# Kernel optimization log

Hardware: AMD Instinct MI355X
Metric: run time of the kernel (lower is better)

## Reference

```python
import jax, jax.numpy as jnp
import numpy as np

S_DIM = 128            # attention head width s
E_DIM = 1024           # expansion e = 2*hidden
SQRT_S = 128.0 ** 0.5
EPS = 1e-5


def setup_inputs() -> dict:
    key = jax.random.key(0)
    ks = jax.random.split(key, 8)
    B, S, H = 64, 512, 512
    uv_dim = 2 * E_DIM + S_DIM  # 2176
    # xavier-uniform-ish scale for uv weight
    lim = (6.0 / (H + uv_dim)) ** 0.5
    return {
        "x": jax.random.normal(ks[0], (B, S, H), dtype=jnp.float32),
        "ln_g": jnp.ones((1,), dtype=jnp.float32),
        "uv_w": jax.random.uniform(ks[1], (uv_dim, H), minval=-lim, maxval=lim, dtype=jnp.float32),
        "uv_b": jnp.zeros((uv_dim,), dtype=jnp.float32),
        "gamma": jax.random.uniform(ks[2], (2, S_DIM), dtype=jnp.float32),
        "beta": jax.random.uniform(ks[3], (2, S_DIM), dtype=jnp.float32),
        "w_bias": jax.random.uniform(ks[4], (2 * S - 1,), dtype=jnp.float32),
        "o_w": jax.random.normal(ks[5], (H, E_DIM), dtype=jnp.float32) * 0.02,
        "o_b": jnp.zeros((H,), dtype=jnp.float32),
    }


def _rope(x):
    # x: [B, S, 2, s]; rotate along the sequence dim (dim=1)
    S = x.shape[1]
    half = x.shape[-1] // 2
    pos = jnp.arange(S, dtype=jnp.float32)
    # torch: freq_seq = -arange(half)/half; inv_freq = 10000**(-freq_seq)
    inv_freq = 10000.0 ** (jnp.arange(half, dtype=jnp.float32) / half)
    sinus = pos[:, None, None] * inv_freq[None, None, :]  # [S, 1, half]
    sin, cos = jnp.sin(sinus), jnp.cos(sinus)
    x1, x2 = x[..., :half], x[..., half:]
    return jnp.concatenate([x1 * cos - x2 * sin, x2 * cos + x1 * sin], axis=-1)


def reference(x, ln_g, uv_w, uv_b, gamma, beta, w_bias, o_w, o_b):
    B, S, H = x.shape
    # ScaleNorm
    norm = jnp.linalg.norm(x, axis=-1, keepdims=True) * (H ** -0.5)
    xn = x / jnp.maximum(norm, EPS) * ln_g
    # fused uv projection + SiLU
    act = jax.nn.silu(xn @ uv_w.T + uv_b)  # [B, S, 2e+s]
    u = act[..., :E_DIM]
    v = act[..., E_DIM:2 * E_DIM]
    base = act[..., 2 * E_DIM:]                      # [B, S, s]
    base = base[:, :, None, :] * gamma + beta        # [B, S, 2, s]
    base = _rope(base)
    q, k = base[:, :, 0, :], base[:, :, 1, :]
    # scores + relative position bias: bias[i, j] = w[j - i + S - 1]
    qk = jnp.einsum('bsd,btd->bst', q, k)
    idx = jnp.arange(S)[None, :] - jnp.arange(S)[:, None] + (S - 1)
    qk = qk + w_bias[idx]
    # relu2 similarity kernel
    kernel = jnp.square(jax.nn.relu(qk / SQRT_S))    # [B, S, S]
    out = u * jnp.einsum('bst,bte->bse', kernel, v)  # gated attention
    out = out @ o_w.T + o_b
    return out + x  # use_shortcut: hidden == output
```

## Files before the change

kernel.cpp:

```cpp
#include <hip/hip_runtime.h>
#include <math.h>


#define M_TOT   32768
#define S_LEN   512
#define H_DIM   512
#define E_DIMC  1024
#define UV_DIM  2176
#define UV_PAD  2304
#define D_DIM   128

using floatx4  = __attribute__((ext_vector_type(4))) float;
using uintx2   = __attribute__((ext_vector_type(2))) unsigned int;
using uintx4   = __attribute__((ext_vector_type(4))) unsigned int;
using ushortx4 = __attribute__((ext_vector_type(4))) unsigned short;
using short8   = __attribute__((ext_vector_type(8))) short;

#define ASYNC_CP16(gsrc, ldst)                                                  \
    __builtin_amdgcn_global_load_lds(                                           \
        (const __attribute__((address_space(1))) void*)(gsrc),                  \
        (__attribute__((address_space(3))) void*)(ldst), 16, 0, 0)

__device__ __forceinline__ float bf2f(unsigned short h) {
    union { unsigned int u; float f; } c;
    c.u = ((unsigned int)h) << 16;
    return c.f;
}
__device__ __forceinline__ unsigned short f2bf(float f) {
    union { float f; unsigned int u; } c;
    c.f = f;
    unsigned int r = c.u + 0x7fffu + ((c.u >> 16) & 1u);
    return (unsigned short)(r >> 16);
}
__device__ __forceinline__ float silu_fast(float x) {
    float e = __expf(-x);
    return x * __builtin_amdgcn_rcpf(1.0f + e);
}
__device__ __forceinline__ int xcd_remap(int b, int nwg) {
    return (b & 7) * (nwg >> 3) + (b >> 3);
}

__global__ __launch_bounds__(256) void f2bf_kernel(const float* __restrict__ in,
                                                   unsigned short* __restrict__ out,
                                                   int n4) {
    int i = blockIdx.x * 256 + threadIdx.x;
    if (i < n4) {
        floatx4 v = ((const floatx4*)in)[i];
        ushortx4 o;
        o.x = f2bf(v.x); o.y = f2bf(v.y); o.z = f2bf(v.z); o.w = f2bf(v.w);
        ((ushortx4*)out)[i] = o;
    }
}

__global__ __launch_bounds__(256) void f2bf_pad_kernel(const float* __restrict__ in,
                                                       unsigned short* __restrict__ out,
                                                       int n4_src, int n4_dst) {
    int i = blockIdx.x * 256 + threadIdx.x;
    if (i < n4_dst) {
        ushortx4 o;
        if (i < n4_src) {
            floatx4 v = ((const floatx4*)in)[i];
            o.x = f2bf(v.x); o.y = f2bf(v.y); o.z = f2bf(v.z); o.w = f2bf(v.w);
        } else {
            o.x = 0; o.y = 0; o.z = 0; o.w = 0;
        }
        ((ushortx4*)out)[i] = o;
    }
}

__global__ __launch_bounds__(256) void rmsnorm_kernel(const float* __restrict__ x,
                                                      const float* __restrict__ ln_g,
                                                      unsigned short* __restrict__ xn) {
    int row  = blockIdx.x * 4 + (threadIdx.x >> 6);
    int lane = threadIdx.x & 63;
    const float* xr = x + (size_t)row * H_DIM;
    floatx4 v0 = ((const floatx4*)xr)[lane];
    floatx4 v1 = ((const floatx4*)xr)[lane + 64];
    float ss = v0.x*v0.x + v0.y*v0.y + v0.z*v0.z + v0.w*v0.w
             + v1.x*v1.x + v1.y*v1.y + v1.z*v1.z + v1.w*v1.w;
    #pragma unroll
    for (int off = 32; off > 0; off >>= 1) ss += __shfl_xor(ss, off, 64);
    float norm = sqrtf(ss) * 0.044194173824159216f;
    float sc   = ln_g[0] / fmaxf(norm, 1e-5f);
    unsigned short* xo = xn + (size_t)row * H_DIM;
    ushortx4 o0, o1;
    o0.x = f2bf(v0.x * sc); o0.y = f2bf(v0.y * sc);
    o0.z = f2bf(v0.z * sc); o0.w = f2bf(v0.w * sc);
    o1.x = f2bf(v1.x * sc); o1.y = f2bf(v1.y * sc);
    o1.z = f2bf(v1.z * sc); o1.w = f2bf(v1.w * sc);
    ((ushortx4*)xo)[lane]      = o0;
    ((ushortx4*)xo)[lane + 64] = o1;
}

__global__ __launch_bounds__(64) void rope_table_kernel(float* __restrict__ cost,
                                                        float* __restrict__ sint) {
    int s = blockIdx.x;
    int j = threadIdx.x;
    float invf = (float)pow(10000.0, (double)j / 64.0);
    float ang  = (float)s * invf;
    double a   = (double)ang;
    cost[s * 64 + j] = (float)cos(a);
    sint[s * 64 + j] = (float)sin(a);
}

__global__ __launch_bounds__(256) void rope_apply_kernel(const float* __restrict__ base,
                                                         const float* __restrict__ gamma,
                                                         const float* __restrict__ beta,
                                                         const float* __restrict__ cost,
                                                         const float* __restrict__ sint,
                                                         unsigned short* __restrict__ q,
                                                         unsigned short* __restrict__ k) {
    int idx = blockIdx.x * 256 + threadIdx.x;
    int m = idx >> 6;
    int j = idx & 63;
    int s = m & (S_LEN - 1);
    float b1 = base[(size_t)m * D_DIM + j];
    float b2 = base[(size_t)m * D_DIM + 64 + j];
    float c  = cost[s * 64 + j];
    float sn = sint[s * 64 + j];
    float yq1 = b1 * gamma[j]       + beta[j];
    float yq2 = b2 * gamma[64 + j]  + beta[64 + j];
    float yk1 = b1 * gamma[128 + j] + beta[128 + j];
    float yk2 = b2 * gamma[192 + j] + beta[192 + j];
    q[(size_t)m * D_DIM + j]      = f2bf(yq1 * c - yq2 * sn);
    q[(size_t)m * D_DIM + 64 + j] = f2bf(yq2 * c + yq1 * sn);
    k[(size_t)m * D_DIM + j]      = f2bf(yk1 * c - yk2 * sn);
    k[(size_t)m * D_DIM + 64 + j] = f2bf(yk2 * c + yk1 * sn);
}

template <bool SWAPT>
__device__ __forceinline__ void gemm128_core(const unsigned short* __restrict__ A,
                                             const unsigned short* __restrict__ B,
                                             int lda, int ldb, int K,
                                             int m0, int n0,
                                             unsigned short (&st)[3][12288],
                                             floatx4 (&acc)[4][4]) {
    const int tid  = threadIdx.x;
    const int lane = tid & 63;
    const int wave = tid >> 6;
    const int quad = lane >> 4;
    const int l16  = lane & 15;
    const int wrow = (wave >> 2) * 64;
    const int wcol = (wave & 3) * 64;

    const int qa  = wave * 64 + lane;
    const int Ra  = qa >> 3;
    const int ca  = (qa & 7) ^ (Ra & 7);
    const int srA = 2 * Ra + (ca >> 2);
    const int scA = (ca & 3) * 8;
    const unsigned short* pa  = A + (size_t)(m0 + srA) * lda + scA;
    const unsigned short* pb0 = B + (size_t)(n0 + srA) * ldb + scA;
    const unsigned short* pb1 = pb0 + (size_t)128 * ldb;
    const int ldsA  = (wave * 64) * 8;
    const int ldsB0 = 4096 + (wave * 64) * 8;
    const int ldsB1 = 4096 + (512 + wave * 64) * 8;

    #pragma unroll
    for (int i = 0; i < 4; i++)
        #pragma unroll
        for (int j = 0; j < 4; j++) acc[i][j] = (floatx4){0.f, 0.f, 0.f, 0.f};

    const int NT = K >> 5;
    auto stage = [&](int buf, int t) {
        unsigned short* s = &st[buf][0];
        const int kt = t * 32;
        ASYNC_CP16(pa  + kt, s + ldsA);
        ASYNC_CP16(pb0 + kt, s + ldsB0);
        ASYNC_CP16(pb1 + kt, s + ldsB1);
    };
    stage(0, 0);
    stage(1, 1);

    int aoff[4], boff[4];
    #pragma unroll
    for (int mt = 0; mt < 4; mt++) {
        int r  = wrow + mt * 16 + l16;
        int Rr = r >> 1;
        int cp = (((r & 1) << 2) + quad) ^ (Rr & 7);
        aoff[mt] = Rr * 64 + cp * 8;
    }
    #pragma unroll
    for (int nt = 0; nt < 4; nt++) {
        int r  = wcol + nt * 16 + l16;
        int Rr = r >> 1;
        int cp = (((r & 1) << 2) + quad) ^ (Rr & 7);
        boff[nt] = 4096 + Rr * 64 + cp * 8;
    }

    int bc = 0, bs = 2;
    for (int t = 0; t < NT; ++t) {
        if (t < NT - 1) asm volatile("s_waitcnt vmcnt(3)" ::: "memory");
        else            asm volatile("s_waitcnt vmcnt(0)" ::: "memory");
        __builtin_amdgcn_sched_barrier(0);
        __builtin_amdgcn_s_barrier();
        __builtin_amdgcn_sched_barrier(0);
        if (t + 2 < NT) stage(bs, t + 2);

        const unsigned short* sb = &st[bc][0];
        short8 af[4], bf[4];
        #pragma unroll
        for (int mt = 0; mt < 4; mt++) {
            union { short8 s8; uintx4 u4; } fu;
            fu.u4 = *(const uintx4*)&sb[aoff[mt]];
            af[mt] = fu.s8;
        }
        #pragma unroll
        for (int nt = 0; nt < 4; nt++) {
            union { short8 s8; uintx4 u4; } fu;
            fu.u4 = *(const uintx4*)&sb[boff[nt]];
            bf[nt] = fu.s8;
        }
        __builtin_amdgcn_s_setprio(1);
        #pragma unroll
        for (int mt = 0; mt < 4; mt++)
            #pragma unroll
            for (int nt = 0; nt < 4; nt++)
                acc[mt][nt] = SWAPT
                    ? __builtin_amdgcn_mfma_f32_16x16x32_bf16(bf[nt], af[mt], acc[mt][nt], 0, 0, 0)
                    : __builtin_amdgcn_mfma_f32_16x16x32_bf16(af[mt], bf[nt], acc[mt][nt], 0, 0, 0);
        __builtin_amdgcn_s_setprio(0);

        bc = (bc == 2) ? 0 : bc + 1;
        bs = (bs == 2) ? 0 : bs + 1;
    }
}

union __align__(16) Lds3 {
    unsigned short st[3][12288];
    unsigned short T[128 * 256];
};

__global__ __launch_bounds__(512, 2) void gemm1_128_kernel(const unsigned short* __restrict__ xn,
                                                           const unsigned short* __restrict__ uvw,
                                                           const float* __restrict__ uvb,
                                                           unsigned short* __restrict__ u,
                                                           unsigned short* __restrict__ vT,
                                                           float* __restrict__ base) {
    __shared__ Lds3 lds;
    floatx4 acc[4][4];
    const int bl = blockIdx.y * 9 + blockIdx.x;
    const int lg = xcd_remap(bl, 9 * (M_TOT / 128));
    const int xb = lg % 9;
    const int m0 = (lg / 9) * 128;
    const int tid = threadIdx.x, lane = tid & 63, wave = tid >> 6;
    const int quad = lane >> 4, l16 = lane & 15;
    const int wrow = (wave >> 2) * 64, wcol = (wave & 3) * 64;

    if (xb < 4) {
        const int n0 = xb * 256;
        gemm128_core<true>(xn, uvw, H_DIM, H_DIM, H_DIM, m0, n0, lds.st, acc);
        __syncthreads();
        #pragma unroll
        for (int mt = 0; mt < 4; mt++) {
            int row = wrow + mt * 16 + l16;
            #pragma unroll
            for (int nt = 0; nt < 4; nt++) {
                int nl = wcol + nt * 16 + quad * 4;
                floatx4 b4 = *(const floatx4*)&uvb[n0 + nl];
                ushortx4 pk;
                #pragma unroll
                for (int r = 0; r < 4; r++)
                    pk[r] = f2bf(silu_fast(acc[mt][nt][r] + b4[r]));
                *(uintx2*)&lds.T[row * 256 + (((nl >> 3) ^ (row & 15)) << 3) + (nl & 7)] = *(uintx2*)&pk;
            }
        }
        __syncthreads();
        #pragma unroll
        for (int i = 0; i < 8; i++) {
            int idx = tid + i * 512;
            int row = idx >> 5, c16 = idx & 31;
            *(uintx4*)(u + (size_t)(m0 + row) * E_DIMC + n0 + c16 * 8) =
                *(const uintx4*)&lds.T[row * 256 + ((c16 ^ (row & 15)) << 3)];
        }
    } else if (xb < 8) {
        const int n0 = xb * 256;
        gemm128_core<false>(xn, uvw, H_DIM, H_DIM, H_DIM, m0, n0, lds.st, acc);
        __syncthreads();
        #pragma unroll
        for (int nt = 0; nt < 4; nt++) {
            int rowT = wcol + nt * 16 + l16;
            float bias = uvb[n0 + rowT];
            #pragma unroll
            for (int mt = 0; mt < 4; mt++) {
                int colT = wrow + mt * 16 + quad * 4;
                ushortx4 pk;
                #pragma unroll
                for (int r = 0; r < 4; r++)
                    pk[r] = f2bf(silu_fast(acc[mt][nt][r] + bias));
                *(uintx2*)&lds.T[rowT * 128 + (((colT >> 3) ^ (rowT & 15)) << 3) + (colT & 7)] = *(uintx2*)&pk;
            }
        }
        __syncthreads();
        const int b = m0 >> 9, sg0 = m0 & (S_LEN - 1), eg0 = n0 - E_DIMC;
        #pragma unroll
        for (int i = 0; i < 8; i++) {
            int idx = tid + i * 512;
            int e = idx >> 4, j = idx & 15;
            *(uintx4*)(vT + ((size_t)b * E_DIMC + eg0 + e) * S_LEN + sg0 + j * 8) =
                *(const uintx4*)&lds.T[e * 128 + ((j ^ (e & 15)) << 3)];
        }
    } else {
        const int n0 = 2048;
        gemm128_core<false>(xn, uvw, H_DIM, H_DIM, H_DIM, m0, n0, lds.st, acc);
        if ((wave & 3) < 2) {
            #pragma unroll
            for (int mt = 0; mt < 4; mt++) {
                int m = m0 + wrow + mt * 16 + quad * 4;
                #pragma unroll
                for (int nt = 0; nt < 4; nt++) {
                    int n = wcol + nt * 16 + l16;
                    float bias = uvb[2048 + n];
                    #pragma unroll
                    for (int r = 0; r < 4; r++)
                        base[(size_t)(m + r) * D_DIM + n] = silu_fast(acc[mt][nt][r] + bias);
                }
            }
        }
    }
}

__global__ __launch_bounds__(512, 2) void gemm_out128_kernel(const unsigned short* __restrict__ oe,
                                                             const unsigned short* __restrict__ ow,
                                                             const float* __restrict__ ob,
                                                             const float* __restrict__ x,
                                                             float* __restrict__ out) {
    __shared__ __align__(16) unsigned short st[3][12288];
    floatx4 acc[4][4];
    const int bl = blockIdx.y * 2 + blockIdx.x;
    const int lg = xcd_remap(bl, 2 * (M_TOT / 128));
    const int n0 = (lg & 1) * 256;
    const int m0 = (lg >> 1) * 128;
    gemm128_core<true>(oe, ow, E_DIMC, E_DIMC, E_DIMC, m0, n0, st, acc);

    const int tid = threadIdx.x, lane = tid & 63, wave = tid >> 6;
    const int quad = lane >> 4, l16 = lane & 15;
    const int wrow = (wave >> 2) * 64, wcol = (wave & 3) * 64;
    #pragma unroll
    for (int mt = 0; mt < 4; mt++) {
        int m = m0 + wrow + mt * 16 + l16;
        #pragma unroll
        for (int nt = 0; nt < 4; nt++) {
            int n = n0 + wcol + nt * 16 + quad * 4;
            size_t off = (size_t)m * H_DIM + n;
            floatx4 b4 = *(const floatx4*)&ob[n];
            floatx4 x4 = *(const floatx4*)&x[off];
            *(floatx4*)&out[off] = acc[mt][nt] + b4 + x4;
        }
    }
}

__global__ __launch_bounds__(512, 2) void gemm_pv128_kernel(const unsigned short* __restrict__ P,
                                                            const unsigned short* __restrict__ vT,
                                                            unsigned short* __restrict__ u) {
    __shared__ Lds3 lds;
    floatx4 acc[4][4];
    const int bl = (blockIdx.z * 4 + blockIdx.y) * 4 + blockIdx.x;
    const int lg = xcd_remap(bl, 1024);
    const int bx = lg & 3, by = (lg >> 2) & 3, bb = lg >> 4;
    const unsigned short* Pb  = P  + (size_t)bb * S_LEN * S_LEN;
    const unsigned short* vTb = vT + (size_t)bb * E_DIMC * S_LEN;
    const int m0 = bx * 128, n0 = by * 256;
    gemm128_core<true>(Pb, vTb, S_LEN, S_LEN, S_LEN, m0, n0, lds.st, acc);

    const int tid = threadIdx.x, lane = tid & 63, wave = tid >> 6;
    const int quad = lane >> 4, l16 = lane & 15;
    const int wrow = (wave >> 2) * 64, wcol = (wave & 3) * 64;
    __syncthreads();
    #pragma unroll
    for (int mt = 0; mt < 4; mt++) {
        int row = wrow + mt * 16 + l16;
        #pragma unroll
        for (int nt = 0; nt < 4; nt++) {
            int nl = wcol + nt * 16 + quad * 4;
            ushortx4 pk;
            #pragma unroll
            for (int r = 0; r < 4; r++) pk[r] = f2bf(acc[mt][nt][r]);
            *(uintx2*)&lds.T[row * 256 + (((nl >> 3) ^ (row & 15)) << 3) + (nl & 7)] = *(uintx2*)&pk;
        }
    }
    __syncthreads();
    #pragma unroll
    for (int i = 0; i < 8; i++) {
        int idx = tid + i * 512;
        int row = idx >> 5, c16 = idx & 31;
        size_t off = ((size_t)bb * S_LEN + m0 + row) * E_DIMC + n0 + c16 * 8;
        union { uintx4 u4; unsigned short s[8]; } tv, uv, ov;
        tv.u4 = *(const uintx4*)&lds.T[row * 256 + ((c16 ^ (row & 15)) << 3)];
        uv.u4 = *(const uintx4*)(u + off);
        #pragma unroll
        for (int jj = 0; jj < 8; jj++) ov.s[jj] = f2bf(bf2f(tv.s[jj]) * bf2f(uv.s[jj]));
        *(uintx4*)(u + off) = ov.u4;
    }
}

struct GemmLds {
    unsigned short As[128 * 64];
    unsigned short Bs[128 * 64];
};

template <bool SWAPT>
__device__ __forceinline__ void gemm_bt_core(const unsigned short* __restrict__ A,
                                             const unsigned short* __restrict__ B,
                                             int lda, int ldb, int K,
                                             int m0, int n0,
                                             GemmLds& lds, floatx4 (&acc)[4][4]) {
    const int tid  = threadIdx.x;
    const int lane = tid & 63;
    const int wave = tid >> 6;
    const int quad = lane >> 4;
    const int l16  = lane & 15;
    const int wm   = (wave >> 1) * 64;
    const int wn   = (wave & 1) * 64;
    const int lrow = lane >> 3;
    const int cgs  = ((lane & 7) ^ lrow) * 8;

    #pragma unroll
    for (int i = 0; i < 4; i++)
        #pragma unroll
        for (int j = 0; j < 4; j++) acc[i][j] = (floatx4){0.f, 0.f, 0.f, 0.f};

    for (int kt = 0; kt < K; kt += 64) {
        #pragma unroll
        for (int i = 0; i < 4; i++) {
            int r0 = wave * 32 + i * 8;
            const unsigned short* ga = A + (size_t)(m0 + r0 + lrow) * lda + kt + cgs;
            const unsigned short* gb = B + (size_t)(n0 + r0 + lrow) * ldb + kt + cgs;
            ASYNC_CP16(ga, &lds.As[r0 * 64]);
            ASYNC_CP16(gb, &lds.Bs[r0 * 64]);
        }
        __syncthreads();
        #pragma unroll
        for (int kk = 0; kk < 64; kk += 32) {
            short8 af[4], bf[4];
            const int pc = (kk + quad * 8) ^ ((l16 & 7) * 8);
            #pragma unroll
            for (int mt = 0; mt < 4; mt++) {
                int row = wm + mt * 16 + l16;
                union { short8 s8; uintx4 u4; } fu;
                fu.u4 = *(const uintx4*)&lds.As[row * 64 + pc];
                af[mt] = fu.s8;
            }
            #pragma unroll
            for (int nt = 0; nt < 4; nt++) {
                int row = wn + nt * 16 + l16;
                union { short8 s8; uintx4 u4; } fu;
                fu.u4 = *(const uintx4*)&lds.Bs[row * 64 + pc];
                bf[nt] = fu.s8;
            }
            #pragma unroll
            for (int mt = 0; mt < 4; mt++)
                #pragma unroll
                for (int nt = 0; nt < 4; nt++)
                    acc[mt][nt] = SWAPT
                        ? __builtin_amdgcn_mfma_f32_16x16x32_bf16(bf[nt], af[mt], acc[mt][nt], 0, 0, 0)
                        : __builtin_amdgcn_mfma_f32_16x16x32_bf16(af[mt], bf[nt], acc[mt][nt], 0, 0, 0);
        }
        __syncthreads();
    }
}

union LdsU {
    GemmLds g;
    unsigned short T[128 * 128];
};
__device__ __forceinline__ int swz(int row, int col) {
    return row * 128 + ((((col >> 3) ^ (row & 7)) << 3) | (col & 7));
}

__global__ __launch_bounds__(256) void gemm_qk_kernel(const unsigned short* __restrict__ q,
                                                      const unsigned short* __restrict__ k,
                                                      const float* __restrict__ wbias,
                                                      unsigned short* __restrict__ P) {
    __shared__ LdsU lds;
    floatx4 acc[4][4];
    const int bl = (blockIdx.z * 4 + blockIdx.y) * 4 + blockIdx.x;
    const int lg = xcd_remap(bl, 1024);
    const int bx = lg & 3, by = (lg >> 2) & 3, bz = lg >> 4;
    size_t boff = (size_t)bz * S_LEN * D_DIM;
    unsigned short* Pb = P + (size_t)bz * S_LEN * S_LEN;
    const int m0 = bx * 128, n0 = by * 128;
    gemm_bt_core<true>(q + boff, k + boff, D_DIM, D_DIM, D_DIM, m0, n0, lds.g, acc);

    const int tid = threadIdx.x, lane = tid & 63, wave = tid >> 6;
    const int quad = lane >> 4, l16 = lane & 15;
    const int wm = (wave >> 1) * 64, wn = (wave & 1) * 64;
    #pragma unroll
    for (int mt = 0; mt < 4; mt++) {
        int row = wm + mt * 16 + l16;
        int s   = m0 + row;
        #pragma unroll
        for (int nt = 0; nt < 4; nt++) {
            int nl = wn + nt * 16 + quad * 4;
            int t0 = n0 + nl;
            ushortx4 pk;
            #pragma unroll
            for (int r = 0; r < 4; r++) {
                float z = (acc[mt][nt][r] + wbias[t0 + r - s + (S_LEN - 1)]) * 0.08838834764831845f;
                z = fmaxf(z, 0.f);
                pk[r] = f2bf(z * z);
            }
            *(uintx2*)&lds.T[swz(row, nl)] = *(uintx2*)&pk;
        }
    }
    __syncthreads();
    #pragma unroll
    for (int i = 0; i < 8; i++) {
        int idx = tid + i * 256;
        int row = idx >> 4;
        int j   = idx & 15;
        *(uintx4*)(Pb + (size_t)(m0 + row) * S_LEN + n0 + j * 8) =
            *(const uintx4*)&lds.T[swz(row, j * 8)];
    }
}

extern "C" void kernel_launch(void* const* d_in, const int* in_sizes, int n_in,
                              void* d_out, int out_size, void* d_ws, size_t ws_size,
                              hipStream_t stream) {
    const float* x     = (const float*)d_in[0];
    const float* ln_g  = (const float*)d_in[1];
    const float* uv_w  = (const float*)d_in[2];
    const float* uv_b  = (const float*)d_in[3];
    const float* gamma = (const float*)d_in[4];
    const float* beta  = (const float*)d_in[5];
    const float* wbias = (const float*)d_in[6];
    const float* o_w   = (const float*)d_in[7];
    const float* o_b   = (const float*)d_in[8];
    float* out = (float*)d_out;

    char* ws = (char*)d_ws;
    size_t off = 0;
    auto alloc = [&](size_t bytes) {
        void* p = ws + off;
        off += (bytes + 255) & ~(size_t)255;
        return p;
    };
    unsigned short* u     = (unsigned short*)alloc((size_t)M_TOT * E_DIMC * 2);
    unsigned short* vT    = (unsigned short*)alloc((size_t)64 * E_DIMC * S_LEN * 2);
    unsigned short* xn    = (unsigned short*)alloc((size_t)M_TOT * H_DIM * 2);
    unsigned short* P     = xn;
    float*          base  = (float*)alloc((size_t)M_TOT * D_DIM * 4);
    unsigned short* q     = (unsigned short*)alloc((size_t)M_TOT * D_DIM * 2);
    unsigned short* k     = (unsigned short*)alloc((size_t)M_TOT * D_DIM * 2);
    float*          cost  = (float*)alloc((size_t)S_LEN * 64 * 4);
    float*          sint  = (float*)alloc((size_t)S_LEN * 64 * 4);
    unsigned short* uvwb  = (unsigned short*)alloc((size_t)UV_PAD * H_DIM * 2);
    unsigned short* owb   = (unsigned short*)alloc((size_t)H_DIM * E_DIMC * 2);
    (void)ws_size; (void)in_sizes; (void)n_in; (void)out_size;

    f2bf_pad_kernel<<<(UV_PAD * H_DIM / 4 + 255) / 256, 256, 0, stream>>>(
        uv_w, uvwb, UV_DIM * H_DIM / 4, UV_PAD * H_DIM / 4);
    f2bf_kernel<<<(H_DIM * E_DIMC / 4 + 255) / 256, 256, 0, stream>>>(o_w, owb, H_DIM * E_DIMC / 4);
    rope_table_kernel<<<S_LEN, 64, 0, stream>>>(cost, sint);

    rmsnorm_kernel<<<M_TOT / 4, 256, 0, stream>>>(x, ln_g, xn);

    gemm1_128_kernel<<<dim3(9, M_TOT / 128), 512, 0, stream>>>(xn, uvwb, uv_b, u, vT, base);

    rope_apply_kernel<<<M_TOT * 64 / 256, 256, 0, stream>>>(base, gamma, beta, cost, sint, q, k);

    gemm_qk_kernel<<<dim3(S_LEN / 128, S_LEN / 128, 64), 256, 0, stream>>>(q, k, wbias, P);

    gemm_pv128_kernel<<<dim3(S_LEN / 128, E_DIMC / 256, 64), 512, 0, stream>>>(P, vT, u);

    gemm_out128_kernel<<<dim3(H_DIM / 256, M_TOT / 128), 512, 0, stream>>>(u, owb, o_b, x, out);
}
```

Before: 365.8 us.

## Shrink GEMM LDS to double buffering and split epilogue staging into halves

The shared 128x256 GEMM core goes from a triple-buffered cp.async pipeline with two stages in flight to a double-buffered one that waits for all loads before each tile. The epilogue transpose buffers are halved, and each kernel now writes its output through LDS in two passes with extra barriers, so the union fits in two stage buffers. The aim is to cut LDS per block from 72KB to 48KB, which could let more blocks share a CU. The cost is less latency hiding, since the prefetch depth drops to one tile and every iteration drains vmcnt, plus extra synchronisation in the epilogue.

```diff
diff --git a/kernel.cpp b/kernel.cpp
--- a/kernel.cpp
+++ b/kernel.cpp
@@ -133,7 +133,7 @@
                                              const unsigned short* __restrict__ B,
                                              int lda, int ldb, int K,
                                              int m0, int n0,
-                                             unsigned short (&st)[3][12288],
+                                             unsigned short (&st)[2][12288],
                                              floatx4 (&acc)[4][4]) {
     const int tid  = threadIdx.x;
     const int lane = tid & 63;
@@ -169,7 +169,6 @@
         ASYNC_CP16(pb1 + kt, s + ldsB1);
     };
     stage(0, 0);
-    stage(1, 1);
 
     int aoff[4], boff[4];
     #pragma unroll
@@ -187,16 +186,14 @@
         boff[nt] = 4096 + Rr * 64 + cp * 8;
     }
 
-    int bc = 0, bs = 2;
     for (int t = 0; t < NT; ++t) {
-        if (t < NT - 1) asm volatile("s_waitcnt vmcnt(3)" ::: "memory");
-        else            asm volatile("s_waitcnt vmcnt(0)" ::: "memory");
+        asm volatile("s_waitcnt vmcnt(0)" ::: "memory");
         __builtin_amdgcn_sched_barrier(0);
         __builtin_amdgcn_s_barrier();
         __builtin_amdgcn_sched_barrier(0);
-        if (t + 2 < NT) stage(bs, t + 2);
-
-        const unsigned short* sb = &st[bc][0];
+        if (t + 1 < NT) stage((t + 1) & 1, t + 1);
+
+        const unsigned short* sb = &st[t & 1][0];
         short8 af[4], bf[4];
         #pragma unroll
         for (int mt = 0; mt < 4; mt++) {
@@ -219,15 +216,12 @@
                     ? __builtin_amdgcn_mfma_f32_16x16x32_bf16(bf[nt], af[mt], acc[mt][nt], 0, 0, 0)
                     : __builtin_amdgcn_mfma_f32_16x16x32_bf16(af[mt], bf[nt], acc[mt][nt], 0, 0, 0);
         __builtin_amdgcn_s_setprio(0);
-
-        bc = (bc == 2) ? 0 : bc + 1;
-        bs = (bs == 2) ? 0 : bs + 1;
-    }
-}
-
-union __align__(16) Lds3 {
-    unsigned short st[3][12288];
-    unsigned short T[128 * 256];
+    }
+}
+
+union __align__(16) Lds2 {
+    unsigned short st[2][12288];
+    unsigned short T2[16384];
 };
 
 __global__ __launch_bounds__(512, 2) void gemm1_128_kernel(const unsigned short* __restrict__ xn,
@@ -236,7 +230,7 @@
                                                            unsigned short* __restrict__ u,
                                                            unsigned short* __restrict__ vT,
                                                            float* __restrict__ base) {
-    __shared__ Lds3 lds;
+    __shared__ Lds2 lds;
     floatx4 acc[4][4];
     const int bl = blockIdx.y * 9 + blockIdx.x;
     const int lg = xcd_remap(bl, 9 * (M_TOT / 128));
@@ -251,53 +245,65 @@
         gemm128_core<true>(xn, uvw, H_DIM, H_DIM, H_DIM, m0, n0, lds.st, acc);
         __syncthreads();
         #pragma unroll
-        for (int mt = 0; mt < 4; mt++) {
-            int row = wrow + mt * 16 + l16;
-            #pragma unroll
-            for (int nt = 0; nt < 4; nt++) {
-                int nl = wcol + nt * 16 + quad * 4;
-                floatx4 b4 = *(const floatx4*)&uvb[n0 + nl];
-                ushortx4 pk;
+        for (int h = 0; h < 2; h++) {
+            if ((wave >> 2) == h) {
                 #pragma unroll
-                for (int r = 0; r < 4; r++)
-                    pk[r] = f2bf(silu_fast(acc[mt][nt][r] + b4[r]));
-                *(uintx2*)&lds.T[row * 256 + (((nl >> 3) ^ (row & 15)) << 3) + (nl & 7)] = *(uintx2*)&pk;
-            }
-        }
-        __syncthreads();
-        #pragma unroll
-        for (int i = 0; i < 8; i++) {
-            int idx = tid + i * 512;
-            int row = idx >> 5, c16 = idx & 31;
-            *(uintx4*)(u + (size_t)(m0 + row) * E_DIMC + n0 + c16 * 8) =
-                *(const uintx4*)&lds.T[row * 256 + ((c16 ^ (row & 15)) << 3)];
+                for (int mt = 0; mt < 4; mt++) {
+                    int row = mt * 16 + l16;
+                    #pragma unroll
+                    for (int nt = 0; nt < 4; nt++) {
+                        int nl = wcol + nt * 16 + quad * 4;
+                        floatx4 b4 = *(const floatx4*)&uvb[n0 + nl];
+                        ushortx4 pk;
+                        #pragma unroll
+                        for (int r = 0; r < 4; r++)
+                            pk[r] = f2bf(silu_fast(acc[mt][nt][r] + b4[r]));
+                        *(uintx2*)&lds.T2[row * 256 + (((nl >> 3) ^ (row & 15)) << 3) + (nl & 7)] = *(uintx2*)&pk;
+                    }
+                }
+            }
+            __syncthreads();
+            #pragma unroll
+            for (int i = 0; i < 4; i++) {
+                int idx = tid + i * 512;
+                int row = idx >> 5, c16 = idx & 31;
+                *(uintx4*)(u + (size_t)(m0 + h * 64 + row) * E_DIMC + n0 + c16 * 8) =
+                    *(const uintx4*)&lds.T2[row * 256 + ((c16 ^ (row & 15)) << 3)];
+            }
+            __syncthreads();
         }
     } else if (xb < 8) {
         const int n0 = xb * 256;
         gemm128_core<false>(xn, uvw, H_DIM, H_DIM, H_DIM, m0, n0, lds.st, acc);
         __syncthreads();
-        #pragma unroll
-        for (int nt = 0; nt < 4; nt++) {
-            int rowT = wcol + nt * 16 + l16;
-            float bias = uvb[n0 + rowT];
-            #pragma unroll
-            for (int mt = 0; mt < 4; mt++) {
-                int colT = wrow + mt * 16 + quad * 4;
-                ushortx4 pk;
+        const int b = m0 >> 9, sg0 = m0 & (S_LEN - 1), eg0 = n0 - E_DIMC;
+        #pragma unroll
+        for (int h = 0; h < 2; h++) {
+            if (((wave & 3) >> 1) == h) {
                 #pragma unroll
-                for (int r = 0; r < 4; r++)
-                    pk[r] = f2bf(silu_fast(acc[mt][nt][r] + bias));
-                *(uintx2*)&lds.T[rowT * 128 + (((colT >> 3) ^ (rowT & 15)) << 3) + (colT & 7)] = *(uintx2*)&pk;
-            }
-        }
-        __syncthreads();
-        const int b = m0 >> 9, sg0 = m0 & (S_LEN - 1), eg0 = n0 - E_DIMC;
-        #pragma unroll
-        for (int i = 0; i < 8; i++) {
-            int idx = tid + i * 512;
-            int e = idx >> 4, j = idx & 15;
-            *(uintx4*)(vT + ((size_t)b * E_DIMC + eg0 + e) * S_LEN + sg0 + j * 8) =
-                *(const uintx4*)&lds.T[e * 128 + ((j ^ (e & 15)) << 3)];
+                for (int nt = 0; nt < 4; nt++) {
+                    int rowL = (wave & 1) * 64 + nt * 16 + l16;
+                    float bias = uvb[n0 + h * 128 + rowL];
+                    #pragma unroll
+                    for (int mt = 0; mt < 4; mt++) {
+                        int colT = wrow + mt * 16 + quad * 4;
+                        ushortx4 pk;
+                        #pragma unroll
+                        for (int r = 0; r < 4; r++)
+                            pk[r] = f2bf(silu_fast(acc[mt][nt][r] + bias));
+                        *(uintx2*)&lds.T2[rowL * 128 + (((colT >> 3) ^ (rowL & 15)) << 3) + (colT & 7)] = *(uintx2*)&pk;
+                    }
+                }
+            }
+            __syncthreads();
+            #pragma unroll
+            for (int i = 0; i < 4; i++) {
+                int idx = tid + i * 512;
+                int e2 = idx >> 4, j = idx & 15;
+                *(uintx4*)(vT + ((size_t)b * E_DIMC + eg0 + h * 128 + e2) * S_LEN + sg0 + j * 8) =
+                    *(const uintx4*)&lds.T2[e2 * 128 + ((j ^ (e2 & 15)) << 3)];
+            }
+            __syncthreads();
         }
     } else {
         const int n0 = 2048;
@@ -324,7 +330,7 @@
                                                              const float* __restrict__ ob,
                                                              const float* __restrict__ x,
                                                              float* __restrict__ out) {
-    __shared__ __align__(16) unsigned short st[3][12288];
+    __shared__ __align__(16) unsigned short st[2][12288];
     floatx4 acc[4][4];
     const int bl = blockIdx.y * 2 + blockIdx.x;
     const int lg = xcd_remap(bl, 2 * (M_TOT / 128));
@@ -352,7 +358,7 @@
 __global__ __launch_bounds__(512, 2) void gemm_pv128_kernel(const unsigned short* __restrict__ P,
                                                             const unsigned short* __restrict__ vT,
                                                             unsigned short* __restrict__ u) {
-    __shared__ Lds3 lds;
+    __shared__ Lds2 lds;
     floatx4 acc[4][4];
     const int bl = (blockIdx.z * 4 + blockIdx.y) * 4 + blockIdx.x;
     const int lg = xcd_remap(bl, 1024);
@@ -364,32 +370,38 @@
 
     const int tid = threadIdx.x, lane = tid & 63, wave = tid >> 6;
     const int quad = lane >> 4, l16 = lane & 15;
-    const int wrow = (wave >> 2) * 64, wcol = (wave & 3) * 64;
+    const int wcol = (wave & 3) * 64;
     __syncthreads();
     #pragma unroll
-    for (int mt = 0; mt < 4; mt++) {
-        int row = wrow + mt * 16 + l16;
-        #pragma unroll
-        for (int nt = 0; nt < 4; nt++) {
-            int nl = wcol + nt * 16 + quad * 4;
-            ushortx4 pk;
-            #pragma unroll
-            for (int r = 0; r < 4; r++) pk[r] = f2bf(acc[mt][nt][r]);
-            *(uintx2*)&lds.T[row * 256 + (((nl >> 3) ^ (row & 15)) << 3) + (nl & 7)] = *(uintx2*)&pk;
-        }
-    }
-    __syncthreads();
-    #pragma unroll
-    for (int i = 0; i < 8; i++) {
-        int idx = tid + i * 512;
-        int row = idx >> 5, c16 = idx & 31;
-        size_t off = ((size_t)bb * S_LEN + m0 + row) * E_DIMC + n0 + c16 * 8;
-        union { uintx4 u4; unsigned short s[8]; } tv, uv, ov;
-        tv.u4 = *(const uintx4*)&lds.T[row * 256 + ((c16 ^ (row & 15)) << 3)];
-        uv.u4 = *(const uintx4*)(u + off);
-        #pragma unroll
-        for (int jj = 0; jj < 8; jj++) ov.s[jj] = f2bf(bf2f(tv.s[jj]) * bf2f(uv.s[jj]));
-        *(uintx4*)(u + off) = ov.u4;
+    for (int h = 0; h < 2; h++) {
+        if ((wave >> 2) == h) {
+            #pragma unroll
+            for (int mt = 0; mt < 4; mt++) {
+                int row = mt * 16 + l16;
+                #pragma unroll
+                for (int nt = 0; nt < 4; nt++) {
+                    int nl = wcol + nt * 16 + quad * 4;
+                    ushortx4 pk;
+                    #pragma unroll
+                    for (int r = 0; r < 4; r++) pk[r] = f2bf(acc[mt][nt][r]);
+                    *(uintx2*)&lds.T2[row * 256 + (((nl >> 3) ^ (row & 15)) << 3) + (nl & 7)] = *(uintx2*)&pk;
+                }
+            }
+        }
+        __syncthreads();
+        #pragma unroll
+        for (int i = 0; i < 4; i++) {
+            int idx = tid + i * 512;
+            int row = idx >> 5, c16 = idx & 31;
+            size_t off = ((size_t)bb * S_LEN + m0 + h * 64 + row) * E_DIMC + n0 + c16 * 8;
+            union { uintx4 u4; unsigned short s[8]; } tv, uv, ov;
+            tv.u4 = *(const uintx4*)&lds.T2[row * 256 + ((c16 ^ (row & 15)) << 3)];
+            uv.u4 = *(const uintx4*)(u + off);
+            #pragma unroll
+            for (int jj = 0; jj < 8; jj++) ov.s[jj] = f2bf(bf2f(tv.s[jj]) * bf2f(uv.s[jj]));
+            *(uintx4*)(u + off) = ov.u4;
+        }
+        __syncthreads();
     }
 }
 
```

After: 394.3 us. +7.8%, slower.
